# Optimization experiments

Measured on AMD Instinct MI355X. Metric: run time of the kernel, lower is better.

## Reference

```python
import jax, jax.numpy as jnp
from jax import lax
import numpy as np

SOFT_LOCAL_MAX_SIZE = 3
PAD = SOFT_LOCAL_MAX_SIZE // 2


def setup_inputs() -> dict:
    key = jax.random.key(0)
    k1, k2 = jax.random.split(key)
    x = jax.random.normal(k1, (16, 64, 256, 256), dtype=jnp.float32)
    W = jax.random.normal(k2, (2, 64), dtype=jnp.float32) * 0.1  # 1x1 conv weight [out_c, in_c]
    b = jnp.zeros((2,), dtype=jnp.float32)
    return {"x": x, "W": W, "b": b}


def reference(x, W, b):
    # 1x1 conv == channel contraction
    y = jnp.einsum('bchw,oc->bohw', x, W) + b[None, :, None, None]
    e = jnp.exp(y)  # [B, 2, H, W]
    # replicate pad + 3x3 box SUM (avg_pool * k^2 == sum over window)
    p = jnp.pad(e, ((0, 0), (0, 0), (PAD, PAD), (PAD, PAD)), mode='edge')
    sum_exp = lax.reduce_window(
        p, jnp.float32(0.0), lax.add,
        window_dimensions=(1, 1, SOFT_LOCAL_MAX_SIZE, SOFT_LOCAL_MAX_SIZE),
        window_strides=(1, 1, 1, 1), padding='VALID')
    sum_exp = jnp.sum(sum_exp, axis=1, keepdims=True)  # channel sum -> [B,1,H,W]
    local_max_score = e / sum_exp
    return local_max_score[:, 0, :, :]  # [B, H, W]
```

## Files before the change

kernel.cpp:

```cpp
#include <hip/hip_runtime.h>
#include <math.h>

#define BB 16
#define CC 64
#define HH 256
#define WW 256
#define HWX (HH * WW)
#define NPIX (BB * HWX)

typedef float f4 __attribute__((ext_vector_type(4)));

__global__ __launch_bounds__(256) void conv_exp_kernel(
    const float* __restrict__ x,
    const float* __restrict__ Wt,
    const float* __restrict__ bias,
    float* __restrict__ e0,
    float* __restrict__ s)
{
    __shared__ float w0[CC];
    __shared__ float w1[CC];
    const int tid = threadIdx.x;
    if (tid < CC) {
        w0[tid] = Wt[tid];
        w1[tid] = Wt[CC + tid];
    }
    __syncthreads();

    const float b0 = bias[0];
    const float b1 = bias[1];

    const long long p4 = (long long)blockIdx.x * blockDim.x + tid;
    const long long base = p4 * 4;
    if (base >= NPIX) return;
    const int bimg = (int)(base >> 16);
    const int q    = (int)(base & 65535);
    const float* xp = x + (long long)bimg * CC * HWX + q;

    f4 a0 = {b0, b0, b0, b0};
    f4 a1 = {b1, b1, b1, b1};

    #pragma unroll 8
    for (int c = 0; c < CC; ++c) {
        const f4 v = __builtin_nontemporal_load((const f4*)(xp + (long long)c * HWX));
        const float wc0 = w0[c];
        const float wc1 = w1[c];
        a0[0] = fmaf(v[0], wc0, a0[0]);
        a0[1] = fmaf(v[1], wc0, a0[1]);
        a0[2] = fmaf(v[2], wc0, a0[2]);
        a0[3] = fmaf(v[3], wc0, a0[3]);
        a1[0] = fmaf(v[0], wc1, a1[0]);
        a1[1] = fmaf(v[1], wc1, a1[1]);
        a1[2] = fmaf(v[2], wc1, a1[2]);
        a1[3] = fmaf(v[3], wc1, a1[3]);
    }

    f4 E0, E1, S;
    E0[0] = __expf(a0[0]); E0[1] = __expf(a0[1]); E0[2] = __expf(a0[2]); E0[3] = __expf(a0[3]);
    E1[0] = __expf(a1[0]); E1[1] = __expf(a1[1]); E1[2] = __expf(a1[2]); E1[3] = __expf(a1[3]);
    S = E0 + E1;

    *(f4*)(e0 + base) = E0;
    *(f4*)(s  + base) = S;
}

__global__ __launch_bounds__(256) void box_div_kernel(
    const float* __restrict__ e0,
    const float* __restrict__ s,
    float* __restrict__ out)
{
    const int t4 = blockIdx.x * blockDim.x + threadIdx.x;
    if (t4 >= NPIX / 4) return;
    const int w4   = t4 & 63;
    const int w    = w4 << 2;
    const int hq   = t4 >> 6;
    const int h    = hq & 255;
    const int bimg = hq >> 8;

    const int hm = (h > 0)       ? h - 1 : 0;
    const int hp = (h < HH - 1)  ? h + 1 : HH - 1;

    const float* sb  = s + (long long)bimg * HWX;
    const float* rmp = sb + hm * WW;
    const float* r0p = sb + h  * WW;
    const float* rpp = sb + hp * WW;

    const f4 V = *(const f4*)(rmp + w) + *(const f4*)(r0p + w) + *(const f4*)(rpp + w);

    const int wl = (w > 0)       ? w - 1 : 0;
    const int wr = (w4 < 63)     ? w + 4 : WW - 1;
    const float L = rmp[wl] + r0p[wl] + rpp[wl];
    const float R = rmp[wr] + r0p[wr] + rpp[wr];

    const f4 E = *(const f4*)(e0 + (long long)t4 * 4);

    f4 o;
    o[0] = E[0] / (L    + V[0] + V[1]);
    o[1] = E[1] / (V[0] + V[1] + V[2]);
    o[2] = E[2] / (V[1] + V[2] + V[3]);
    o[3] = E[3] / (V[2] + V[3] + R);

    __builtin_nontemporal_store(o, (f4*)(out + (long long)t4 * 4));
}

extern "C" void kernel_launch(void* const* d_in, const int* in_sizes, int n_in,
                              void* d_out, int out_size, void* d_ws, size_t ws_size,
                              hipStream_t stream) {
    const float* x    = (const float*)d_in[0];
    const float* Wt   = (const float*)d_in[1];
    const float* bias = (const float*)d_in[2];
    float* out = (float*)d_out;

    float* e0 = (float*)d_ws;
    float* s  = e0 + NPIX;

    {
        const int threads = 256;
        const int total = NPIX / 4;
        const int blocks = (total + threads - 1) / threads;
        conv_exp_kernel<<<blocks, threads, 0, stream>>>(x, Wt, bias, e0, s);
    }
    {
        const int threads = 256;
        const int total = NPIX / 4;
        const int blocks = (total + threads - 1) / threads;
        box_div_kernel<<<blocks, threads, 0, stream>>>(e0, s, out);
    }
}
```

Measured before the change: 343.9 us.

## Fuse conv-exp and 3x3 box-normalize into one row-tiled kernel with LDS halo

Merges the two kernels into one. Each block computes a 16-row tile plus halo rows of the channel-reduced exp values, stores the channel-summed exp in shared memory, then does the 3x3 box sum and division from LDS. This removes the workspace round trip and the second launch. In exchange it recomputes the halo rows and launches only 256 blocks, so occupancy is much lower for a bandwidth-heavy load loop.

```diff
diff --git a/kernel.cpp b/kernel.cpp
--- a/kernel.cpp
+++ b/kernel.cpp
@@ -7,18 +7,21 @@
 #define WW 256
 #define HWX (HH * WW)
 #define NPIX (BB * HWX)
+#define TR 16
+#define SR (TR + 2)
 
 typedef float f4 __attribute__((ext_vector_type(4)));
 
-__global__ __launch_bounds__(256) void conv_exp_kernel(
+__global__ __launch_bounds__(256) void fused_kernel(
     const float* __restrict__ x,
     const float* __restrict__ Wt,
     const float* __restrict__ bias,
-    float* __restrict__ e0,
-    float* __restrict__ s)
+    float* __restrict__ out)
 {
     __shared__ float w0[CC];
     __shared__ float w1[CC];
+    __shared__ float s_lds[SR][WW];
+
     const int tid = threadIdx.x;
     if (tid < CC) {
         w0[tid] = Wt[tid];
@@ -29,77 +32,79 @@
     const float b0 = bias[0];
     const float b1 = bias[1];
 
-    const long long p4 = (long long)blockIdx.x * blockDim.x + tid;
-    const long long base = p4 * 4;
-    if (base >= NPIX) return;
-    const int bimg = (int)(base >> 16);
-    const int q    = (int)(base & 65535);
-    const float* xp = x + (long long)bimg * CC * HWX + q;
+    const int blk  = blockIdx.x;
+    const int bimg = blk >> 4;
+    const int tile = blk & 15;
+    const int r0   = tile * TR;
 
-    f4 a0 = {b0, b0, b0, b0};
-    f4 a1 = {b1, b1, b1, b1};
+    const int lane = tid & 63;
+    const int wid  = tid >> 6;
+    const int w    = lane << 2;
 
-    #pragma unroll 8
-    for (int c = 0; c < CC; ++c) {
-        const f4 v = __builtin_nontemporal_load((const f4*)(xp + (long long)c * HWX));
-        const float wc0 = w0[c];
-        const float wc1 = w1[c];
-        a0[0] = fmaf(v[0], wc0, a0[0]);
-        a0[1] = fmaf(v[1], wc0, a0[1]);
-        a0[2] = fmaf(v[2], wc0, a0[2]);
-        a0[3] = fmaf(v[3], wc0, a0[3]);
-        a1[0] = fmaf(v[0], wc1, a1[0]);
-        a1[1] = fmaf(v[1], wc1, a1[1]);
-        a1[2] = fmaf(v[2], wc1, a1[2]);
-        a1[3] = fmaf(v[3], wc1, a1[3]);
+    const float* xb = x + (long long)bimg * CC * HWX;
+
+    f4 e0reg[5];
+
+    #pragma unroll
+    for (int p = 0; p < 5; ++p) {
+        const int lr = (p < 4) ? (4 * p + wid) : (16 + wid);
+        const bool active = (p < 4) || (wid < 2);
+        if (active) {
+            const int rr = r0 - 1 + lr;
+            const int rc = min(max(rr, 0), HH - 1);
+            const float* xp = xb + rc * WW + w;
+            f4 a0 = {b0, b0, b0, b0};
+            f4 a1 = {b1, b1, b1, b1};
+            #pragma unroll 8
+            for (int c = 0; c < CC; ++c) {
+                const f4 v = __builtin_nontemporal_load((const f4*)(xp + (long long)c * HWX));
+                const float wc0 = w0[c];
+                const float wc1 = w1[c];
+                a0[0] = fmaf(v[0], wc0, a0[0]);
+                a0[1] = fmaf(v[1], wc0, a0[1]);
+                a0[2] = fmaf(v[2], wc0, a0[2]);
+                a0[3] = fmaf(v[3], wc0, a0[3]);
+                a1[0] = fmaf(v[0], wc1, a1[0]);
+                a1[1] = fmaf(v[1], wc1, a1[1]);
+                a1[2] = fmaf(v[2], wc1, a1[2]);
+                a1[3] = fmaf(v[3], wc1, a1[3]);
+            }
+            f4 E0, E1;
+            E0[0] = __expf(a0[0]); E0[1] = __expf(a0[1]);
+            E0[2] = __expf(a0[2]); E0[3] = __expf(a0[3]);
+            E1[0] = __expf(a1[0]); E1[1] = __expf(a1[1]);
+            E1[2] = __expf(a1[2]); E1[3] = __expf(a1[3]);
+            e0reg[p] = E0;
+            *(f4*)&s_lds[lr][w] = E0 + E1;
+        }
     }
+    __syncthreads();
 
-    f4 E0, E1, S;
-    E0[0] = __expf(a0[0]); E0[1] = __expf(a0[1]); E0[2] = __expf(a0[2]); E0[3] = __expf(a0[3]);
-    E1[0] = __expf(a1[0]); E1[1] = __expf(a1[1]); E1[2] = __expf(a1[2]); E1[3] = __expf(a1[3]);
-    S = E0 + E1;
+    float* ob = out + (long long)bimg * HWX;
+    const int wl = (w > 0)    ? w - 1 : 0;
+    const int wr = (lane < 63) ? w + 4 : WW - 1;
 
-    *(f4*)(e0 + base) = E0;
-    *(f4*)(s  + base) = S;
-}
-
-__global__ __launch_bounds__(256) void box_div_kernel(
-    const float* __restrict__ e0,
-    const float* __restrict__ s,
-    float* __restrict__ out)
-{
-    const int t4 = blockIdx.x * blockDim.x + threadIdx.x;
-    if (t4 >= NPIX / 4) return;
-    const int w4   = t4 & 63;
-    const int w    = w4 << 2;
-    const int hq   = t4 >> 6;
-    const int h    = hq & 255;
-    const int bimg = hq >> 8;
-
-    const int hm = (h > 0)       ? h - 1 : 0;
-    const int hp = (h < HH - 1)  ? h + 1 : HH - 1;
-
-    const float* sb  = s + (long long)bimg * HWX;
-    const float* rmp = sb + hm * WW;
-    const float* r0p = sb + h  * WW;
-    const float* rpp = sb + hp * WW;
-
-    const f4 V = *(const f4*)(rmp + w) + *(const f4*)(r0p + w) + *(const f4*)(rpp + w);
-
-    const int wl = (w > 0)       ? w - 1 : 0;
-    const int wr = (w4 < 63)     ? w + 4 : WW - 1;
-    const float L = rmp[wl] + r0p[wl] + rpp[wl];
-    const float R = rmp[wr] + r0p[wr] + rpp[wr];
-
-    const f4 E = *(const f4*)(e0 + (long long)t4 * 4);
-
-    f4 o;
-    o[0] = E[0] / (L    + V[0] + V[1]);
-    o[1] = E[1] / (V[0] + V[1] + V[2]);
-    o[2] = E[2] / (V[1] + V[2] + V[3]);
-    o[3] = E[3] / (V[2] + V[3] + R);
-
-    __builtin_nontemporal_store(o, (f4*)(out + (long long)t4 * 4));
+    #pragma unroll
+    for (int p = 0; p < 5; ++p) {
+        const int lr = (p < 4) ? (4 * p + wid) : (16 + wid);
+        const bool isout = (p < 4) ? (lr >= 1) : (wid == 0);
+        if (isout) {
+            const int rr = r0 - 1 + lr;
+            const float* rm = s_lds[lr - 1];
+            const float* rc = s_lds[lr];
+            const float* rp = s_lds[lr + 1];
+            const f4 V = *(const f4*)(rm + w) + *(const f4*)(rc + w) + *(const f4*)(rp + w);
+            const float L = rm[wl] + rc[wl] + rp[wl];
+            const float R = rm[wr] + rc[wr] + rp[wr];
+            const f4 E = e0reg[p];
+            f4 o;
+            o[0] = E[0] / (L    + V[0] + V[1]);
+            o[1] = E[1] / (V[0] + V[1] + V[2]);
+            o[2] = E[2] / (V[1] + V[2] + V[3]);
+            o[3] = E[3] / (V[2] + V[3] + R);
+            __builtin_nontemporal_store(o, (f4*)(ob + rr * WW + w));
+        }
+    }
 }
 
 extern "C" void kernel_launch(void* const* d_in, const int* in_sizes, int n_in,
@@ -109,20 +114,9 @@
     const float* Wt   = (const float*)d_in[1];
     const float* bias = (const float*)d_in[2];
     float* out = (float*)d_out;
+    (void)d_ws; (void)ws_size;
 
-    float* e0 = (float*)d_ws;
-    float* s  = e0 + NPIX;
-
-    {
-        const int threads = 256;
-        const int total = NPIX / 4;
-        const int blocks = (total + threads - 1) / threads;
-        conv_exp_kernel<<<blocks, threads, 0, stream>>>(x, Wt, bias, e0, s);
-    }
-    {
-        const int threads = 256;
-        const int total = NPIX / 4;
-        const int blocks = (total + threads - 1) / threads;
-        box_div_kernel<<<blocks, threads, 0, stream>>>(e0, s, out);
-    }
+    const int threads = 256;
+    const int blocks  = BB * (HH / TR);
+    fused_kernel<<<blocks, threads, 0, stream>>>(x, Wt, bias, out);
 }
```

Measured after the change: 354.6 us. +3.1%, slower.
